# Kernel optimization log

Measured on AMD Instinct MI355X. Metric: run time of the kernel, lower is better.

## Reference

```python
import jax, jax.numpy as jnp
import numpy as np

TOPK = 2
EPS = float(np.finfo(np.float64).eps)


def setup_inputs() -> dict:
    key = jax.random.key(0)
    ks = jax.random.split(key, 6)
    B, D, E = 8192, 1024, 8
    x = jax.random.normal(ks[0], (B, D), dtype=jnp.float32)
    noise = jax.random.normal(ks[1], (B, E), dtype=jnp.float32)
    w_gate = jax.random.normal(ks[2], (D, E), dtype=jnp.float32) * 0.02
    w_noise = jax.random.normal(ks[3], (D, E), dtype=jnp.float32) * 0.02
    W_experts = jax.random.normal(ks[4], (E, D, D), dtype=jnp.float32) * 0.02
    b_experts = jax.random.normal(ks[5], (E, D), dtype=jnp.float32) * 0.02
    return {"x": x, "noise": noise, "w_gate": w_gate, "w_noise": w_noise,
            "W_experts": W_experts, "b_experts": b_experts}


def _gates(x, w_gate, w_noise, noise):
    # noisy top-k gating (Shazeer et al.)
    clean_logits = x @ w_gate                                  # [B, E]
    noise_stddev = jax.nn.softplus(x @ w_noise) + 0.01         # [B, E]
    logits = clean_logits + noise * noise_stddev               # [B, E]
    E = logits.shape[1]
    top_logits, top_idx = jax.lax.top_k(logits, min(TOPK + 1, E))
    top_k_logits = top_logits[:, :TOPK]
    top_k_idx = top_idx[:, :TOPK]
    top_k_gates = jax.nn.softmax(top_k_logits, axis=1)         # [B, k]
    B = logits.shape[0]
    gates = jnp.zeros_like(logits).at[jnp.arange(B)[:, None], top_k_idx].set(top_k_gates)
    return gates                                               # [B, E] sparse


def reference(x, noise, w_gate, w_noise, W_experts, b_experts):
    gates = _gates(x, w_gate, w_noise, noise)                  # [B, E]
    # dense equivalent of sort-based dispatch/combine: zero gates mask out
    # unselected experts, so the combined result is identical math.
    expert_out = jnp.einsum("bd,edh->beh", x, W_experts) + b_experts[None]  # [B, E, D]
    combined = jnp.einsum("be,beh->bh", gates, jnp.exp(expert_out))         # [B, D]
    combined = jnp.where(combined == 0, EPS, combined)
    return jnp.log(combined)
```

## Files before the change

kernel.cpp:

```cpp
#include <hip/hip_runtime.h>
#include <hip/hip_bf16.h>
#include <math.h>

#define B_ROWS 8192
#define DDIM   1024
#define NEXP   8

typedef __attribute__((ext_vector_type(8))) __bf16 bf16x8;
typedef __attribute__((ext_vector_type(4))) float  f32x4;

__device__ __forceinline__ unsigned short f2bf(float f) {
    unsigned u = __builtin_bit_cast(unsigned, f);
    u = (u + 0x7fffu + ((u >> 16) & 1u)) >> 16;
    return (unsigned short)u;
}

__global__ __launch_bounds__(512) void gating_kernel(
    const float* __restrict__ x, const float* __restrict__ noise,
    const float* __restrict__ w_gate, const float* __restrict__ w_noise,
    int* __restrict__ counts, int* __restrict__ rowlist, float* __restrict__ gatelist)
{
    __shared__ double sacc[8][16][16];

    const int t  = threadIdx.x;
    const int kh = t >> 6;
    const int r  = (t >> 2) & 15;
    const int cg = t & 3;
    const int b  = blockIdx.x * 16 + r;

    const float* wbase = (cg < 2) ? w_gate : w_noise;
    const float* wr    = wbase + (cg & 1) * 4;
    const float* xr    = x + (size_t)b * DDIM + kh * 128;

    double a0 = 0.0, a1 = 0.0, a2 = 0.0, a3 = 0.0;
#pragma unroll 4
    for (int k4 = 0; k4 < 32; ++k4) {
        const float4 xv = *(const float4*)(xr + k4 * 4);
        const float xs[4] = {xv.x, xv.y, xv.z, xv.w};
#pragma unroll
        for (int j = 0; j < 4; ++j) {
            const float4 wv = *(const float4*)(wr + (size_t)(kh * 128 + k4 * 4 + j) * NEXP);
            a0 += (double)(xs[j] * wv.x);
            a1 += (double)(xs[j] * wv.y);
            a2 += (double)(xs[j] * wv.z);
            a3 += (double)(xs[j] * wv.w);
        }
    }
    const int c0 = cg * 4;
    sacc[kh][r][c0 + 0] = a0;
    sacc[kh][r][c0 + 1] = a1;
    sacc[kh][r][c0 + 2] = a2;
    sacc[kh][r][c0 + 3] = a3;
    __syncthreads();

    if (t < 256) {
        const int rr = t >> 4;
        const int c  = t & 15;
        const int bb = blockIdx.x * 16 + rr;

        double v = 0.0;
#pragma unroll
        for (int q = 0; q < 8; ++q) v += sacc[q][rr][c];

        const double vnoise = __shfl_xor(v, 8);

        double lgv = -1.0e300;
        if (c < 8) {
            const double z  = vnoise;
            const double sp = (z > 30.0) ? z : log1p(exp(z));
            lgv = v + (double)noise[(size_t)bb * NEXP + c] * (sp + 0.01);
        }

        double bv = lgv; int bi = c;
#pragma unroll
        for (int off = 1; off <= 4; off <<= 1) {
            const double ov = __shfl_xor(bv, off);
            const int    oi = __shfl_xor(bi, off);
            if (ov > bv || (ov == bv && oi < bi)) { bv = ov; bi = oi; }
        }
        double lg2 = (c == bi) ? -1.0e300 : lgv;
        double b2v = lg2; int b2i = c;
#pragma unroll
        for (int off = 1; off <= 4; off <<= 1) {
            const double ov = __shfl_xor(b2v, off);
            const int    oi = __shfl_xor(b2i, off);
            if (ov > b2v || (ov == b2v && oi < b2i)) { b2v = ov; b2i = oi; }
        }

        if (c == 0) {
            const double l0 = bv, l1 = b2v;
            const int    i0 = bi, i1 = b2i;
            const double g0 = 1.0 / (1.0 + exp(l1 - l0));
            const double g1 = 1.0 - g0;

            int p0 = atomicAdd(&counts[i0], 1);
            rowlist [i0 * B_ROWS + p0] = bb;
            gatelist[i0 * B_ROWS + p0] = (float)g0;
            int p1 = atomicAdd(&counts[i1], 1);
            rowlist [i1 * B_ROWS + p1] = bb;
            gatelist[i1 * B_ROWS + p1] = (float)g1;
        }
    }
}

__global__ __launch_bounds__(256) void moe_gemm_kernel(
    const float* __restrict__ x, const float* __restrict__ W,
    const float* __restrict__ bias,
    const int* __restrict__ counts, const int* __restrict__ rowlist,
    const float* __restrict__ gatelist, float* __restrict__ out)
{
    const int e  = blockIdx.z;
    const int mt = blockIdx.y;
    const int nt = blockIdx.x;
    const int cnt  = counts[e];
    const int row0 = mt * 128;
    if (row0 >= cnt) return;

    __shared__ int   srow[128];
    __shared__ float sgate[128];
    __shared__ __align__(16) unsigned char Alds[128 * 64 * 2];
    __shared__ __align__(16) unsigned char Blds[128 * 64 * 2];

    const int t = threadIdx.x;
    if (t < 128) {
        const int r = row0 + t;
        if (r < cnt) { srow[t] = rowlist[e * B_ROWS + r]; sgate[t] = gatelist[e * B_ROWS + r]; }
        else         { srow[t] = 0;                       sgate[t] = 0.0f; }
    }
    __syncthreads();

    const int wave = t >> 6, lane = t & 63;
    const int wr = wave >> 1, wc = wave & 1;
    const int l4 = lane >> 4, l16 = lane & 15;

    f32x4 acc[4][4];
#pragma unroll
    for (int m = 0; m < 4; ++m)
#pragma unroll
        for (int n = 0; n < 4; ++n) acc[m][n] = (f32x4){0.f, 0.f, 0.f, 0.f};

    const float* We = W + (size_t)e * DDIM * DDIM + (size_t)nt * 128;

    for (int kt = 0; kt < DDIM / 64; ++kt) {
#pragma unroll
        for (int c = 0; c < 4; ++c) {
            const int idx = t + c * 256;
            const int row = idx >> 3, k8 = idx & 7;
            const float* src = x + (size_t)srow[row] * DDIM + kt * 64 + k8 * 8;
            const float4 f0 = *(const float4*)src;
            const float4 f1 = *(const float4*)(src + 4);
            union { bf16x8 v; unsigned short u[8]; } pk;
            pk.u[0] = f2bf(f0.x); pk.u[1] = f2bf(f0.y); pk.u[2] = f2bf(f0.z); pk.u[3] = f2bf(f0.w);
            pk.u[4] = f2bf(f1.x); pk.u[5] = f2bf(f1.y); pk.u[6] = f2bf(f1.z); pk.u[7] = f2bf(f1.w);
            *(bf16x8*)(Alds + row * 128 + ((k8 * 16) ^ ((row & 7) << 4))) = pk.v;
        }
#pragma unroll
        for (int c = 0; c < 4; ++c) {
            const int idx = t + c * 256;
            const int n = idx & 127, kc = idx >> 7;
            const float* src = We + (size_t)(kt * 64 + kc * 8) * DDIM + n;
            union { bf16x8 v; unsigned short u[8]; } pk;
#pragma unroll
            for (int j = 0; j < 8; ++j) pk.u[j] = f2bf(src[(size_t)j * DDIM]);
            *(bf16x8*)(Blds + n * 128 + ((kc * 16) ^ ((n & 7) << 4))) = pk.v;
        }
        __syncthreads();

#pragma unroll
        for (int ks = 0; ks < 2; ++ks) {
            bf16x8 af[4], bf[4];
#pragma unroll
            for (int m = 0; m < 4; ++m) {
                const int row = wr * 64 + m * 16 + l16;
                af[m] = *(const bf16x8*)(Alds + row * 128 + ((ks * 64 + l4 * 16) ^ ((row & 7) << 4)));
            }
#pragma unroll
            for (int n = 0; n < 4; ++n) {
                const int rn = wc * 64 + n * 16 + l16;
                bf[n] = *(const bf16x8*)(Blds + rn * 128 + ((ks * 64 + l4 * 16) ^ ((rn & 7) << 4)));
            }
#pragma unroll
            for (int m = 0; m < 4; ++m)
#pragma unroll
                for (int n = 0; n < 4; ++n)
                    acc[m][n] = __builtin_amdgcn_mfma_f32_16x16x32_bf16(af[m], bf[n], acc[m][n], 0, 0, 0);
        }
        __syncthreads();
    }

#pragma unroll
    for (int m = 0; m < 4; ++m) {
#pragma unroll
        for (int n = 0; n < 4; ++n) {
#pragma unroll
            for (int j = 0; j < 4; ++j) {
                const int R = wr * 64 + m * 16 + l4 * 4 + j;
                if (row0 + R < cnt) {
                    const int   brow = srow[R];
                    const float g    = sgate[R];
                    const int   h    = nt * 128 + wc * 64 + n * 16 + l16;
                    const float v    = g * __expf(acc[m][n][j] + bias[e * DDIM + h]);
                    unsafeAtomicAdd(out + (size_t)brow * DDIM + h, v);
                }
            }
        }
    }
}

__global__ __launch_bounds__(256) void logeps_kernel(float* __restrict__ o, int n4)
{
    const float EPSF = 2.220446049250313e-16f;
    int i = blockIdx.x * blockDim.x + threadIdx.x;
    const int stride = gridDim.x * blockDim.x;
    float4* p = (float4*)o;
    for (; i < n4; i += stride) {
        float4 v = p[i];
        v.x = __logf(v.x == 0.0f ? EPSF : v.x);
        v.y = __logf(v.y == 0.0f ? EPSF : v.y);
        v.z = __logf(v.z == 0.0f ? EPSF : v.z);
        v.w = __logf(v.w == 0.0f ? EPSF : v.w);
        p[i] = v;
    }
}

extern "C" void kernel_launch(void* const* d_in, const int* in_sizes, int n_in,
                              void* d_out, int out_size, void* d_ws, size_t ws_size,
                              hipStream_t stream)
{
    const float* x       = (const float*)d_in[0];
    const float* noise   = (const float*)d_in[1];
    const float* w_gate  = (const float*)d_in[2];
    const float* w_noise = (const float*)d_in[3];
    const float* W       = (const float*)d_in[4];
    const float* bias    = (const float*)d_in[5];
    float* out = (float*)d_out;

    char* ws = (char*)d_ws;
    int*   counts   = (int*)ws;
    int*   rowlist  = (int*)(ws + 64);
    float* gatelist = (float*)(ws + 64 + NEXP * B_ROWS * 4);

    hipMemsetAsync(counts, 0, 64, stream);
    hipMemsetAsync(d_out, 0, (size_t)out_size * sizeof(float), stream);

    gating_kernel<<<B_ROWS / 16, 512, 0, stream>>>(x, noise, w_gate, w_noise,
                                                   counts, rowlist, gatelist);

    dim3 grid(NEXP, B_ROWS / 128, NEXP);
    moe_gemm_kernel<<<grid, 256, 0, stream>>>(x, W, bias, counts, rowlist, gatelist, out);

    logeps_kernel<<<2048, 256, 0, stream>>>(out, out_size / 4);
}
```

Baseline: 396.0 us.

## Pre-convert x and W to bf16 and stream tiles via global_load_lds

Adds two pre-pass kernels: one converts x to bf16 and one transposes each expert's weight matrix into a K-contiguous bf16 layout. The MoE GEMM can then load A and B tiles straight into LDS with 16-byte global_load_lds instead of converting fp32 values in registers and reading W with strided scalar loads. The gating kernel is also restructured so the gate and noise weights sit in shared memory and each lane accumulates one full-length column. The cost is two extra passes over x and W (including 32 MB of W reads) and more workspace, and the GEMM main loop still has no double buffering.

```diff
diff --git a/kernel.cpp b/kernel.cpp
--- a/kernel.cpp
+++ b/kernel.cpp
@@ -15,96 +15,141 @@
     return (unsigned short)u;
 }
 
-__global__ __launch_bounds__(512) void gating_kernel(
+#define GLOAD_LDS16(gptr, lptr)                                                \
+    __builtin_amdgcn_global_load_lds(                                          \
+        (const __attribute__((address_space(1))) unsigned int*)(gptr),         \
+        (__attribute__((address_space(3))) unsigned int*)(lptr), 16, 0, 0)
+
+__global__ __launch_bounds__(256) void xconv_kernel(
+    const float* __restrict__ x, __hip_bfloat16* __restrict__ xbf)
+{
+    int i = blockIdx.x * 256 + threadIdx.x;
+    const int stride = gridDim.x * 256;
+    const int n8 = B_ROWS * DDIM / 8;
+    for (; i < n8; i += stride) {
+        const float4 f0 = *(const float4*)(x + (size_t)i * 8);
+        const float4 f1 = *(const float4*)(x + (size_t)i * 8 + 4);
+        union { bf16x8 v; unsigned short u[8]; } pk;
+        pk.u[0] = f2bf(f0.x); pk.u[1] = f2bf(f0.y); pk.u[2] = f2bf(f0.z); pk.u[3] = f2bf(f0.w);
+        pk.u[4] = f2bf(f1.x); pk.u[5] = f2bf(f1.y); pk.u[6] = f2bf(f1.z); pk.u[7] = f2bf(f1.w);
+        *(bf16x8*)((__hip_bfloat16*)xbf + (size_t)i * 8) = pk.v;
+    }
+}
+
+__global__ __launch_bounds__(256) void wtrans_kernel(
+    const float* __restrict__ W, __hip_bfloat16* __restrict__ Wt)
+{
+    const int e  = blockIdx.z;
+    const int k0 = blockIdx.y * 64;
+    const int n0 = blockIdx.x * 64;
+    __shared__ float st[64][65];
+
+    const int t = threadIdx.x;
+    {
+        const int kk = t >> 4;
+        const int nn = (t & 15) * 4;
+#pragma unroll
+        for (int p = 0; p < 4; ++p) {
+            const int k = p * 16 + kk;
+            const float4 v = *(const float4*)(W + (size_t)e * DDIM * DDIM
+                                                + (size_t)(k0 + k) * DDIM + n0 + nn);
+            st[k][nn + 0] = v.x; st[k][nn + 1] = v.y;
+            st[k][nn + 2] = v.z; st[k][nn + 3] = v.w;
+        }
+    }
+    __syncthreads();
+    {
+        const int wave = t >> 6, lane = t & 63;
+        const int nr = lane >> 3, kc = lane & 7;
+#pragma unroll
+        for (int p = 0; p < 2; ++p) {
+            const int n = p * 32 + wave * 8 + nr;
+            union { bf16x8 v; unsigned short u[8]; } pk;
+#pragma unroll
+            for (int j = 0; j < 8; ++j) pk.u[j] = f2bf(st[kc * 8 + j][n]);
+            *(bf16x8*)((__hip_bfloat16*)Wt + (size_t)e * DDIM * DDIM
+                        + (size_t)(n0 + n) * DDIM + k0 + kc * 8) = pk.v;
+        }
+    }
+}
+
+__global__ __launch_bounds__(256) void gating_kernel(
     const float* __restrict__ x, const float* __restrict__ noise,
     const float* __restrict__ w_gate, const float* __restrict__ w_noise,
     int* __restrict__ counts, int* __restrict__ rowlist, float* __restrict__ gatelist)
 {
-    __shared__ double sacc[8][16][16];
-
-    const int t  = threadIdx.x;
-    const int kh = t >> 6;
-    const int r  = (t >> 2) & 15;
-    const int cg = t & 3;
-    const int b  = blockIdx.x * 16 + r;
-
-    const float* wbase = (cg < 2) ? w_gate : w_noise;
-    const float* wr    = wbase + (cg & 1) * 4;
-    const float* xr    = x + (size_t)b * DDIM + kh * 128;
-
-    double a0 = 0.0, a1 = 0.0, a2 = 0.0, a3 = 0.0;
+    __shared__ float wtab[DDIM][16];
+
+    const int t = threadIdx.x;
+    {
+        const int k0 = t * 4;
+#pragma unroll
+        for (int kk = 0; kk < 4; ++kk) {
+            const float4 g0 = *(const float4*)(w_gate  + (size_t)(k0 + kk) * NEXP);
+            const float4 g1 = *(const float4*)(w_gate  + (size_t)(k0 + kk) * NEXP + 4);
+            const float4 n0 = *(const float4*)(w_noise + (size_t)(k0 + kk) * NEXP);
+            const float4 n1 = *(const float4*)(w_noise + (size_t)(k0 + kk) * NEXP + 4);
+            *(float4*)&wtab[k0 + kk][0]  = g0;
+            *(float4*)&wtab[k0 + kk][4]  = g1;
+            *(float4*)&wtab[k0 + kk][8]  = n0;
+            *(float4*)&wtab[k0 + kk][12] = n1;
+        }
+    }
+    __syncthreads();
+
+    const int wave = t >> 6, lane = t & 63;
+    const int rs = lane >> 4, c = lane & 15;
+    const int row = (blockIdx.x * 4 + wave) * 4 + rs;
+
+    double acc = 0.0;
+    const float* xr = x + (size_t)row * DDIM;
 #pragma unroll 4
-    for (int k4 = 0; k4 < 32; ++k4) {
+    for (int k4 = 0; k4 < DDIM / 4; ++k4) {
         const float4 xv = *(const float4*)(xr + k4 * 4);
-        const float xs[4] = {xv.x, xv.y, xv.z, xv.w};
-#pragma unroll
-        for (int j = 0; j < 4; ++j) {
-            const float4 wv = *(const float4*)(wr + (size_t)(kh * 128 + k4 * 4 + j) * NEXP);
-            a0 += (double)(xs[j] * wv.x);
-            a1 += (double)(xs[j] * wv.y);
-            a2 += (double)(xs[j] * wv.z);
-            a3 += (double)(xs[j] * wv.w);
-        }
-    }
-    const int c0 = cg * 4;
-    sacc[kh][r][c0 + 0] = a0;
-    sacc[kh][r][c0 + 1] = a1;
-    sacc[kh][r][c0 + 2] = a2;
-    sacc[kh][r][c0 + 3] = a3;
-    __syncthreads();
-
-    if (t < 256) {
-        const int rr = t >> 4;
-        const int c  = t & 15;
-        const int bb = blockIdx.x * 16 + rr;
-
-        double v = 0.0;
-#pragma unroll
-        for (int q = 0; q < 8; ++q) v += sacc[q][rr][c];
-
-        const double vnoise = __shfl_xor(v, 8);
-
-        double lgv = -1.0e300;
-        if (c < 8) {
-            const double z  = vnoise;
-            const double sp = (z > 30.0) ? z : log1p(exp(z));
-            lgv = v + (double)noise[(size_t)bb * NEXP + c] * (sp + 0.01);
-        }
-
-        double bv = lgv; int bi = c;
-#pragma unroll
-        for (int off = 1; off <= 4; off <<= 1) {
-            const double ov = __shfl_xor(bv, off);
-            const int    oi = __shfl_xor(bi, off);
-            if (ov > bv || (ov == bv && oi < bi)) { bv = ov; bi = oi; }
-        }
-        double lg2 = (c == bi) ? -1.0e300 : lgv;
-        double b2v = lg2; int b2i = c;
-#pragma unroll
-        for (int off = 1; off <= 4; off <<= 1) {
-            const double ov = __shfl_xor(b2v, off);
-            const int    oi = __shfl_xor(b2i, off);
-            if (ov > b2v || (ov == b2v && oi < b2i)) { b2v = ov; b2i = oi; }
-        }
-
-        if (c == 0) {
-            const double l0 = bv, l1 = b2v;
-            const int    i0 = bi, i1 = b2i;
-            const double g0 = 1.0 / (1.0 + exp(l1 - l0));
-            const double g1 = 1.0 - g0;
-
-            int p0 = atomicAdd(&counts[i0], 1);
-            rowlist [i0 * B_ROWS + p0] = bb;
-            gatelist[i0 * B_ROWS + p0] = (float)g0;
-            int p1 = atomicAdd(&counts[i1], 1);
-            rowlist [i1 * B_ROWS + p1] = bb;
-            gatelist[i1 * B_ROWS + p1] = (float)g1;
-        }
+        acc += (double)(xv.x * wtab[k4 * 4 + 0][c]);
+        acc += (double)(xv.y * wtab[k4 * 4 + 1][c]);
+        acc += (double)(xv.z * wtab[k4 * 4 + 2][c]);
+        acc += (double)(xv.w * wtab[k4 * 4 + 3][c]);
+    }
+
+    const double vnoise = __shfl_xor(acc, 8);
+
+    double lgv = -1.0e300;
+    if (c < 8) {
+        const double z  = vnoise;
+        const double sp = (z > 30.0) ? z : log1p(exp(z));
+        lgv = acc + (double)noise[(size_t)row * NEXP + c] * (sp + 0.01);
+    }
+
+    double bv = lgv; int bi = c;
+#pragma unroll
+    for (int off = 1; off <= 4; off <<= 1) {
+        const double ov = __shfl_xor(bv, off);
+        const int    oi = __shfl_xor(bi, off);
+        if (ov > bv || (ov == bv && oi < bi)) { bv = ov; bi = oi; }
+    }
+    double b2v = (c == bi) ? -1.0e300 : lgv; int b2i = c;
+#pragma unroll
+    for (int off = 1; off <= 4; off <<= 1) {
+        const double ov = __shfl_xor(b2v, off);
+        const int    oi = __shfl_xor(b2i, off);
+        if (ov > b2v || (ov == b2v && oi < b2i)) { b2v = ov; b2i = oi; }
+    }
+
+    if (c == 0) {
+        const double g0 = 1.0 / (1.0 + exp(b2v - bv));
+        const double g1 = 1.0 - g0;
+        int p0 = atomicAdd(&counts[bi], 1);
+        rowlist [bi * B_ROWS + p0] = row;
+        gatelist[bi * B_ROWS + p0] = (float)g0;
+        int p1 = atomicAdd(&counts[b2i], 1);
+        rowlist [b2i * B_ROWS + p1] = row;
+        gatelist[b2i * B_ROWS + p1] = (float)g1;
     }
 }
 
 __global__ __launch_bounds__(256) void moe_gemm_kernel(
-    const float* __restrict__ x, const float* __restrict__ W,
+    const __hip_bfloat16* __restrict__ xbf, const __hip_bfloat16* __restrict__ Wt,
     const float* __restrict__ bias,
     const int* __restrict__ counts, const int* __restrict__ rowlist,
     const float* __restrict__ gatelist, float* __restrict__ out)
@@ -118,20 +163,31 @@
 
     __shared__ int   srow[128];
     __shared__ float sgate[128];
-    __shared__ __align__(16) unsigned char Alds[128 * 64 * 2];
-    __shared__ __align__(16) unsigned char Blds[128 * 64 * 2];
+    __shared__ __align__(16) unsigned char Alds[128 * 128];
+    __shared__ __align__(16) unsigned char Blds[128 * 128];
 
     const int t = threadIdx.x;
     if (t < 128) {
         const int r = row0 + t;
-        if (r < cnt) { srow[t] = rowlist[e * B_ROWS + r]; sgate[t] = gatelist[e * B_ROWS + r]; }
-        else         { srow[t] = 0;                       sgate[t] = 0.0f; }
+        srow[t]  = (r < cnt) ? rowlist[e * B_ROWS + r]  : 0;
+        sgate[t] = (r < cnt) ? gatelist[e * B_ROWS + r] : 0.0f;
     }
     __syncthreads();
 
     const int wave = t >> 6, lane = t & 63;
     const int wr = wave >> 1, wc = wave & 1;
     const int l4 = lane >> 4, l16 = lane & 15;
+    const int lrow  = lane >> 3;
+    const int lchunk = (lane & 7) ^ lrow;
+
+    const char* asrc[4]; const char* bsrc[4];
+#pragma unroll
+    for (int i = 0; i < 4; ++i) {
+        const int r  = wave * 32 + i * 8 + lrow;
+        asrc[i] = (const char*)xbf + 2 * ((size_t)srow[r] * DDIM + lchunk * 8);
+        const int gn = nt * 128 + wave * 32 + i * 8 + lrow;
+        bsrc[i] = (const char*)Wt  + 2 * ((size_t)e * DDIM * DDIM + (size_t)gn * DDIM + lchunk * 8);
+    }
 
     f32x4 acc[4][4];
 #pragma unroll
@@ -139,36 +195,19 @@
 #pragma unroll
         for (int n = 0; n < 4; ++n) acc[m][n] = (f32x4){0.f, 0.f, 0.f, 0.f};
 
-    const float* We = W + (size_t)e * DDIM * DDIM + (size_t)nt * 128;
-
     for (int kt = 0; kt < DDIM / 64; ++kt) {
-#pragma unroll
-        for (int c = 0; c < 4; ++c) {
-            const int idx = t + c * 256;
-            const int row = idx >> 3, k8 = idx & 7;
-            const float* src = x + (size_t)srow[row] * DDIM + kt * 64 + k8 * 8;
-            const float4 f0 = *(const float4*)src;
-            const float4 f1 = *(const float4*)(src + 4);
-            union { bf16x8 v; unsigned short u[8]; } pk;
-            pk.u[0] = f2bf(f0.x); pk.u[1] = f2bf(f0.y); pk.u[2] = f2bf(f0.z); pk.u[3] = f2bf(f0.w);
-            pk.u[4] = f2bf(f1.x); pk.u[5] = f2bf(f1.y); pk.u[6] = f2bf(f1.z); pk.u[7] = f2bf(f1.w);
-            *(bf16x8*)(Alds + row * 128 + ((k8 * 16) ^ ((row & 7) << 4))) = pk.v;
-        }
-#pragma unroll
-        for (int c = 0; c < 4; ++c) {
-            const int idx = t + c * 256;
-            const int n = idx & 127, kc = idx >> 7;
-            const float* src = We + (size_t)(kt * 64 + kc * 8) * DDIM + n;
-            union { bf16x8 v; unsigned short u[8]; } pk;
-#pragma unroll
-            for (int j = 0; j < 8; ++j) pk.u[j] = f2bf(src[(size_t)j * DDIM]);
-            *(bf16x8*)(Blds + n * 128 + ((kc * 16) ^ ((n & 7) << 4))) = pk.v;
-        }
+        const int koff = kt * 128;
+#pragma unroll
+        for (int i = 0; i < 4; ++i) {
+            GLOAD_LDS16(asrc[i] + koff, Alds + (wave * 32 + i * 8) * 128);
+            GLOAD_LDS16(bsrc[i] + koff, Blds + (wave * 32 + i * 8) * 128);
+        }
+        asm volatile("s_waitcnt vmcnt(0)" ::: "memory");
         __syncthreads();
 
 #pragma unroll
         for (int ks = 0; ks < 2; ++ks) {
-            bf16x8 af[4], bf[4];
+            bf16x8 af[4], bfr[4];
 #pragma unroll
             for (int m = 0; m < 4; ++m) {
                 const int row = wr * 64 + m * 16 + l16;
@@ -177,13 +216,13 @@
 #pragma unroll
             for (int n = 0; n < 4; ++n) {
                 const int rn = wc * 64 + n * 16 + l16;
-                bf[n] = *(const bf16x8*)(Blds + rn * 128 + ((ks * 64 + l4 * 16) ^ ((rn & 7) << 4)));
+                bfr[n] = *(const bf16x8*)(Blds + rn * 128 + ((ks * 64 + l4 * 16) ^ ((rn & 7) << 4)));
             }
 #pragma unroll
             for (int m = 0; m < 4; ++m)
 #pragma unroll
                 for (int n = 0; n < 4; ++n)
-                    acc[m][n] = __builtin_amdgcn_mfma_f32_16x16x32_bf16(af[m], bf[n], acc[m][n], 0, 0, 0);
+                    acc[m][n] = __builtin_amdgcn_mfma_f32_16x16x32_bf16(af[m], bfr[n], acc[m][n], 0, 0, 0);
         }
         __syncthreads();
     }
@@ -237,17 +276,21 @@
 
     char* ws = (char*)d_ws;
     int*   counts   = (int*)ws;
-    int*   rowlist  = (int*)(ws + 64);
-    float* gatelist = (float*)(ws + 64 + NEXP * B_ROWS * 4);
+    int*   rowlist  = (int*)(ws + 1024);
+    float* gatelist = (float*)(ws + 1024 + NEXP * B_ROWS * 4);
+    __hip_bfloat16* xbf = (__hip_bfloat16*)(ws + (1u << 20));
+    __hip_bfloat16* Wt  = (__hip_bfloat16*)(ws + (1u << 20) + (16u << 20));
 
     hipMemsetAsync(counts, 0, 64, stream);
     hipMemsetAsync(d_out, 0, (size_t)out_size * sizeof(float), stream);
 
-    gating_kernel<<<B_ROWS / 16, 512, 0, stream>>>(x, noise, w_gate, w_noise,
+    xconv_kernel<<<1024, 256, 0, stream>>>(x, xbf);
+    wtrans_kernel<<<dim3(16, 16, NEXP), 256, 0, stream>>>(W, Wt);
+    gating_kernel<<<B_ROWS / 16, 256, 0, stream>>>(x, noise, w_gate, w_noise,
                                                    counts, rowlist, gatelist);
 
     dim3 grid(NEXP, B_ROWS / 128, NEXP);
-    moe_gemm_kernel<<<grid, 256, 0, stream>>>(x, W, bias, counts, rowlist, gatelist, out);
+    moe_gemm_kernel<<<grid, 256, 0, stream>>>(xbf, Wt, bias, counts, rowlist, gatelist, out);
 
     logeps_kernel<<<2048, 256, 0, stream>>>(out, out_size / 4);
 }
```

New measurement: 368.1 us. 7.0% less time.
